# Kernel tuning notes

Measured on AMD Instinct MI355X. Metric: run time of the kernel, lower is better.

## Reference

```python
import jax, jax.numpy as jnp
import numpy as np

B, C, ANGRES, H, W = 4, 60, 5, 96, 96
N = ANGRES * ANGRES  # 25 angular views
D = C                # dims = channels in TrippleAttention


def _norm(x, axis):
    # torch F.normalize: x / max(||x||_2, 1e-12)
    n = jnp.linalg.norm(x, axis=axis, keepdims=True)
    return x / jnp.maximum(n, 1e-12)


def setup_inputs() -> dict:
    key = jax.random.key(0)
    ks = jax.random.split(key, 8)
    s = 0.02
    return {
        "x": jax.random.normal(ks[0], (B, C, N, H, W), jnp.float32),
        "w_spa_q": jax.random.normal(ks[1], (D, C), jnp.float32) * s,      # 1x1 conv, stride 1
        "w_spa_kv": jax.random.normal(ks[2], (2 * D, C), jnp.float32) * s, # 1x1 conv, stride 2
        "w_ang_qkv": jax.random.normal(ks[3], (3 * D, C), jnp.float32) * s,
        "w_fre_qkv": jax.random.normal(ks[4], (3 * D, C), jnp.float32) * s,
        "ln_gamma": jnp.ones((3 * D,), jnp.float32),
        "ln_beta": jnp.zeros((3 * D,), jnp.float32),
        "w_mlp1": jax.random.normal(ks[5], (C, 3 * D), jnp.float32) * s,   # torch Linear [out,in]
        "w_mlp2": jax.random.normal(ks[6], (C, C), jnp.float32) * s,
    }


def reference(x, w_spa_q, w_spa_kv, w_ang_qkv, w_fre_qkv, ln_gamma, ln_beta, w_mlp1, w_mlp2):
    b, c, n, h, w = x.shape
    d = w_spa_q.shape[0]

    # ---- SpatialAttention ----
    # q: stride-1 1x1 conv then '(b n) c h w -> b (h w) (c n)'
    sq = jnp.einsum('dc,bcnhw->bhwdn', w_spa_q, x).reshape(b, h * w, d * n)
    xs = x[:, :, :, ::2, ::2]                       # stride-2, kernel-1 conv == subsample
    h2, w2 = xs.shape[3], xs.shape[4]
    skv = jnp.einsum('dc,bcnhw->bdnhw', w_spa_kv, xs)
    sk = skv[:, :d].reshape(b, d * n, h2 * w2)       # 'b (c n) (h w)'
    sv = skv[:, d:].transpose(0, 3, 4, 1, 2).reshape(b, h2 * w2, d * n)  # 'b (h w) (c n)'
    sq = _norm(sq, -1)
    sk = _norm(sk, -2)
    s_att = jax.nn.softmax(sq @ sk, axis=-1)         # [b, hw, h2w2]
    s_fea = (s_att @ sv).reshape(b, h, w, d, n).transpose(0, 3, 4, 1, 2)  # [b,d,n,h,w]

    # ---- AngularAttention ----
    aqkv = jnp.einsum('dc,bcnhw->bdnhw', w_ang_qkv, x)
    aq = aqkv[:, :d].transpose(0, 2, 1, 3, 4).reshape(b, n, d * h * w)       # 'b (u v) (c h w)'
    ak = aqkv[:, d:2 * d].transpose(0, 1, 3, 4, 2).reshape(b, d * h * w, n)  # 'b (c h w) (u v)'
    av = aqkv[:, 2 * d:].transpose(0, 2, 1, 3, 4).reshape(b, n, d * h * w)
    aq = _norm(aq, -1)
    ak = _norm(ak, -2)
    a_att = jax.nn.softmax(aq @ ak, axis=-1)         # [b, n, n]
    a_fea = (a_att @ av).reshape(b, n, d, h, w).transpose(0, 2, 1, 3, 4)     # [b,d,n,h,w]

    # ---- FrequencyAttention (use_mask=False) ----
    fqkv = jnp.einsum('dc,bcnhw->bdnhw', w_fre_qkv, x)
    fq = fqkv[:, :d].reshape(b, d, n * h * w)        # 'b c (n h w)'
    fk = fqkv[:, d:2 * d].reshape(b, d, n * h * w).transpose(0, 2, 1)        # 'b (n h w) c'
    fv = fqkv[:, 2 * d:].reshape(b, d, n * h * w)
    fq = _norm(fq, -1)
    fk = _norm(fk, -2)
    f_att = jax.nn.softmax(fq @ fk, axis=-1)         # [b, d, d]
    f_fea = (f_att @ fv).reshape(b, d, n, h, w)

    # ---- concat + MLP (dropout is identity at inference) ----
    cat = jnp.concatenate([s_fea, a_fea, f_fea], axis=1)  # [b, 3d, n, h, w]
    t = cat.transpose(0, 3, 4, 2, 1)                      # [b, h, w, n, 3d]
    mu = t.mean(-1, keepdims=True)
    var = t.var(-1, keepdims=True)                        # biased var, matching torch LayerNorm
    t = (t - mu) / jnp.sqrt(var + 1e-5) * ln_gamma + ln_beta
    t = jax.nn.relu(t @ w_mlp1.T)
    t = t @ w_mlp2.T                                      # [b, h, w, n, c]
    return t.transpose(0, 4, 3, 1, 2) + x
```

## Files before the change

### kernel.cpp

```cpp
#include <hip/hip_runtime.h>
#include <hip/hip_bf16.h>

typedef unsigned short u16;
typedef float f32x4 __attribute__((ext_vector_type(4)));
typedef short s16x8 __attribute__((ext_vector_type(8)));


__device__ __forceinline__ float b2f(u16 u) {
  union { unsigned int i; float f; } v; v.i = ((unsigned int)u) << 16; return v.f;
}
__device__ __forceinline__ u16 f2b(float f) {
  union { float f; unsigned int i; } v; v.f = f;
  unsigned int i = v.i + 0x7FFFu + ((v.i >> 16) & 1u);
  return (u16)(i >> 16);
}

__global__ void fallback_copy(const float* __restrict__ x, float* __restrict__ out, size_t n) {
  size_t i = (size_t)blockIdx.x * 256 + threadIdx.x;
  size_t st = (size_t)gridDim.x * 256;
  for (; i < n; i += st) out[i] = x[i];
}

__global__ __launch_bounds__(256) void cast_x(const float* __restrict__ xb, u16* __restrict__ Xb) {
  size_t e = ((size_t)blockIdx.x * 256 + threadIdx.x) * 4;
  ushort4 o;
  if (e < 13824000) {
    float4 v = *(const float4*)(xb + e);
    o.x = f2b(v.x); o.y = f2b(v.y); o.z = f2b(v.z); o.w = f2b(v.w);
  } else { o.x = 0; o.y = 0; o.z = 0; o.w = 0; }
  *(ushort4*)(Xb + e) = o;
}

__global__ __launch_bounds__(256) void gram_gemm(const u16* __restrict__ Xall,
                                                 float* __restrict__ Pg) {
  __shared__ __align__(16) u16 As[128 * 40];
  __shared__ __align__(16) u16 Bs[128 * 40];
  const int z = blockIdx.z;
  const int b = z >> 1, kk = z & 1;
  const u16* A = Xall + (size_t)b * 14155776;
  float* C = Pg + (size_t)z * 2359296;
  const int tid = threadIdx.x;
  const int bm = blockIdx.x, bn = blockIdx.y;
  const int lane = tid & 63;
  const int wv = tid >> 6;
  const int wm = (wv >> 1) * 64, wn = (wv & 1) * 64;
  const int lm = lane & 15, lq = lane >> 4;
  f32x4 z4 = {0.f, 0.f, 0.f, 0.f};
  f32x4 acc[4][4];
#pragma unroll
  for (int i = 0; i < 4; ++i)
#pragma unroll
    for (int j = 0; j < 4; ++j) acc[i][j] = z4;

  const int kbeg = kk * 4608, kend = kbeg + 4608;
  for (int k0 = kbeg; k0 < kend; k0 += 32) {
    __syncthreads();
#pragma unroll
    for (int r = 0; r < 4; ++r) {
      int idx = tid + (r << 8);
      int row = (idx >> 2) & 127;
      int seg = idx & 3;
      if (r < 2) {
        const uint4* src = (const uint4*)(A + (size_t)(bm * 128 + row) * 9216 + k0 + seg * 8);
        *(uint4*)&As[row * 40 + seg * 8] = *src;
      } else {
        const uint4* src = (const uint4*)(A + (size_t)(bn * 128 + row) * 9216 + k0 + seg * 8);
        *(uint4*)&Bs[row * 40 + seg * 8] = *src;
      }
    }
    __syncthreads();
    s16x8 af[4], bf[4];
#pragma unroll
    for (int i = 0; i < 4; ++i)
      af[i] = *(const s16x8*)&As[(wm + i * 16 + lm) * 40 + lq * 8];
#pragma unroll
    for (int j = 0; j < 4; ++j)
      bf[j] = *(const s16x8*)&Bs[(wn + j * 16 + lm) * 40 + lq * 8];
#pragma unroll
    for (int i = 0; i < 4; ++i)
#pragma unroll
      for (int j = 0; j < 4; ++j)
        acc[i][j] = __builtin_amdgcn_mfma_f32_16x16x32_bf16(af[i], bf[j], acc[i][j], 0, 0, 0);
  }

#pragma unroll
  for (int i = 0; i < 4; ++i) {
    int row0 = bm * 128 + wm + i * 16 + lq * 4;
#pragma unroll
    for (int j = 0; j < 4; ++j) {
      int col = bn * 128 + wn + j * 16 + lm;
#pragma unroll
      for (int r = 0; r < 4; ++r)
        C[(size_t)(row0 + r) * 1536 + col] = acc[i][j][r];
    }
  }
}

__global__ __launch_bounds__(256) void reduce_g2(const float* __restrict__ Pg,
                                                 float* __restrict__ G2all) {
  int b = blockIdx.y;
  size_t r = ((size_t)blockIdx.x * 256 + threadIdx.x) * 4;
  float4 a = *(const float4*)(Pg + (size_t)(2 * b) * 2359296 + r);
  float4 c = *(const float4*)(Pg + (size_t)(2 * b + 1) * 2359296 + r);
  float4 o; o.x = a.x + c.x; o.y = a.y + c.y; o.z = a.z + c.z; o.w = a.w + c.w;
  *(float4*)(G2all + (size_t)b * 2359296 + r) = o;
}

__global__ __launch_bounds__(256) void proj_full(const float* __restrict__ xb,
    const float* __restrict__ Wq, const float* __restrict__ Wang,
    const float* __restrict__ Wfre, u16* __restrict__ PF) {
  int s = blockIdx.x * 256 + threadIdx.x;
  int grp = blockIdx.y;
  const float* W = (grp == 0) ? Wq : ((grp == 1) ? (Wang + 7200) : (Wfre + 7200));
  const float* xs = xb + s;
  float xr[60];
#pragma unroll
  for (int c = 0; c < 60; ++c) xr[c] = xs[(size_t)c * 230400];
  u16* ob = PF + (size_t)grp * 13824000 + s;
  for (int r0 = 0; r0 < 60; r0 += 4) {
    const float* w0 = W + r0 * 60;
    const float* w1 = w0 + 60;
    const float* w2 = w0 + 120;
    const float* w3 = w0 + 180;
    float a0 = 0.f, a1 = 0.f, a2 = 0.f, a3 = 0.f;
#pragma unroll
    for (int c = 0; c < 60; ++c) {
      float xv = xr[c];
      a0 += w0[c] * xv; a1 += w1[c] * xv; a2 += w2[c] * xv; a3 += w3[c] * xv;
    }
    ob[(size_t)(r0    ) * 230400] = f2b(a0);
    ob[(size_t)(r0 + 1) * 230400] = f2b(a1);
    ob[(size_t)(r0 + 2) * 230400] = f2b(a2);
    ob[(size_t)(r0 + 3) * 230400] = f2b(a3);
  }
}

__global__ __launch_bounds__(256) void proj_sub(const float* __restrict__ xb,
    const float* __restrict__ Wkv, u16* __restrict__ PS) {
  int s2 = blockIdx.x * 256 + threadIdx.x;
  int grp = blockIdx.y;
  int nn = s2 / 2304; int rem = s2 - nn * 2304;
  int hy = rem / 48;  int hx = rem - hy * 48;
  const float* xs = xb + (size_t)nn * 9216 + hy * 192 + hx * 2;
  float xr[60];
#pragma unroll
  for (int c = 0; c < 60; ++c) xr[c] = xs[(size_t)c * 230400];
  u16* ob = PS + (size_t)grp * 1728000 + s2;
  const float* Wg = Wkv + grp * 1800;
  for (int r0 = 0; r0 < 30; r0 += 5) {
    const float* w0 = Wg + r0 * 60;
    const float* w1 = w0 + 60;
    const float* w2 = w0 + 120;
    const float* w3 = w0 + 180;
    const float* w4 = w0 + 240;
    float a0 = 0.f, a1 = 0.f, a2 = 0.f, a3 = 0.f, a4 = 0.f;
#pragma unroll
    for (int c = 0; c < 60; ++c) {
      float xv = xr[c];
      a0 += w0[c] * xv; a1 += w1[c] * xv; a2 += w2[c] * xv;
      a3 += w3[c] * xv; a4 += w4[c] * xv;
    }
    ob[(size_t)(r0    ) * 57600] = f2b(a0);
    ob[(size_t)(r0 + 1) * 57600] = f2b(a1);
    ob[(size_t)(r0 + 2) * 57600] = f2b(a2);
    ob[(size_t)(r0 + 3) * 57600] = f2b(a3);
    ob[(size_t)(r0 + 4) * 57600] = f2b(a4);
  }
}

__global__ __launch_bounds__(256) void norm_sums(const u16* __restrict__ inb,
    float* __restrict__ partials, int S) {
  int s = blockIdx.x * 256 + threadIdx.x;
  int fc = blockIdx.y;
  const u16* p = inb + (size_t)(fc * 60) * S + s;
  float a0 = 0.f, a1 = 0.f, a2 = 0.f, a3 = 0.f;
#pragma unroll
  for (int f = 0; f < 60; f += 4) {
    float v0 = b2f(p[(size_t)(f + 0) * S]); a0 += v0 * v0;
    float v1 = b2f(p[(size_t)(f + 1) * S]); a1 += v1 * v1;
    float v2 = b2f(p[(size_t)(f + 2) * S]); a2 += v2 * v2;
    float v3 = b2f(p[(size_t)(f + 3) * S]); a3 += v3 * v3;
  }
  partials[(size_t)fc * S + s] = (a0 + a1) + (a2 + a3);
}

__global__ __launch_bounds__(256) void transpose_scale(const u16* __restrict__ inb,
    const float* __restrict__ partials, u16* __restrict__ outb, int S) {
  __shared__ float Ts[64 * 65];
  __shared__ float rinv[64];
  int s0 = blockIdx.x * 64, f0 = blockIdx.y * 64;
  int t = threadIdx.x; int sl = t & 63; int g = t >> 6;
  if (t < 64) {
    float tot = 0.f;
    for (int c = 0; c < 25; ++c) tot += partials[(size_t)c * S + s0 + t];
    rinv[t] = 1.f / fmaxf(sqrtf(tot), 1e-12f);
  }
  for (int e = t; e < 4096; e += 256) {
    int fr = e >> 6, sc = e & 63; int f = f0 + fr;
    Ts[fr * 65 + sc] = (f < 1500) ? b2f(inb[(size_t)f * S + s0 + sc]) : 0.f;
  }
  __syncthreads();
  for (int sr = g; sr < 64; sr += 4) {
    float v = Ts[sl * 65 + sr] * rinv[sr];
    outb[(size_t)(s0 + sr) * 1536 + f0 + sl] = f2b(v);
  }
}

template<int M, int N, int K, int EPI>
__global__ __launch_bounds__(256) void gemm_bt(const u16* __restrict__ A,
    const u16* __restrict__ BT, void* __restrict__ C) {
  __shared__ __align__(16) u16 As[128 * 40];
  __shared__ __align__(16) u16 Bs[128 * 40];
  const int tid = threadIdx.x;
  const int bm = blockIdx.x, bn = blockIdx.y;
  const int lane = tid & 63;
  const int wv = tid >> 6;
  const int wm = (wv >> 1) * 64, wn = (wv & 1) * 64;
  const int lm = lane & 15, lq = lane >> 4;
  f32x4 z = {0.f, 0.f, 0.f, 0.f};
  f32x4 acc[4][4];
#pragma unroll
  for (int i = 0; i < 4; ++i)
#pragma unroll
    for (int j = 0; j < 4; ++j) acc[i][j] = z;

  for (int k0 = 0; k0 < K; k0 += 32) {
    __syncthreads();
#pragma unroll
    for (int r = 0; r < 4; ++r) {
      int idx = tid + (r << 8);
      int row = (idx >> 2) & 127;
      int seg = idx & 3;
      if (r < 2) {
        const uint4* src = (const uint4*)(A + (size_t)(bm * 128 + row) * K + k0 + seg * 8);
        *(uint4*)&As[row * 40 + seg * 8] = *src;
      } else {
        const uint4* src = (const uint4*)(BT + (size_t)(bn * 128 + row) * K + k0 + seg * 8);
        *(uint4*)&Bs[row * 40 + seg * 8] = *src;
      }
    }
    __syncthreads();
    s16x8 af[4], bf[4];
#pragma unroll
    for (int i = 0; i < 4; ++i)
      af[i] = *(const s16x8*)&As[(wm + i * 16 + lm) * 40 + lq * 8];
#pragma unroll
    for (int j = 0; j < 4; ++j)
      bf[j] = *(const s16x8*)&Bs[(wn + j * 16 + lm) * 40 + lq * 8];
#pragma unroll
    for (int i = 0; i < 4; ++i)
#pragma unroll
      for (int j = 0; j < 4; ++j)
        acc[i][j] = __builtin_amdgcn_mfma_f32_16x16x32_bf16(af[i], bf[j], acc[i][j], 0, 0, 0);
  }

#pragma unroll
  for (int i = 0; i < 4; ++i) {
    int row0 = bm * 128 + wm + i * 16 + lq * 4;
#pragma unroll
    for (int j = 0; j < 4; ++j) {
      int col = bn * 128 + wn + j * 16 + lm;
      if (EPI == 0) {
        float* Cb = (float*)C;
#pragma unroll
        for (int r = 0; r < 4; ++r)
          Cb[(size_t)(row0 + r) * N + col] = acc[i][j][r];
      } else {
        if (col < 1500) {
          u16* Cb = (u16*)C;
          uint2 pk;
          pk.x = (unsigned int)f2b(acc[i][j][0]) | ((unsigned int)f2b(acc[i][j][1]) << 16);
          pk.y = (unsigned int)f2b(acc[i][j][2]) | ((unsigned int)f2b(acc[i][j][3]) << 16);
          *(uint2*)&Cb[(size_t)col * M + row0] = pk;
        }
      }
    }
  }
}

__global__ __launch_bounds__(256) void softmax_rows(const float* __restrict__ L,
                                                    u16* __restrict__ att) {
  size_t row = blockIdx.x;
  const float* Lr = L + row * 2304;
  u16* ar = att + row * 2304;
  int t = threadIdx.x;
  float v[9]; float mx = -1e30f;
#pragma unroll
  for (int i = 0; i < 9; ++i) { v[i] = Lr[t + i * 256]; mx = fmaxf(mx, v[i]); }
  __shared__ float red[256];
  red[t] = mx; __syncthreads();
  for (int st = 128; st > 0; st >>= 1) { if (t < st) red[t] = fmaxf(red[t], red[t + st]); __syncthreads(); }
  mx = red[0]; __syncthreads();
  float s = 0.f;
#pragma unroll
  for (int i = 0; i < 9; ++i) { v[i] = __expf(v[i] - mx); s += v[i]; }
  red[t] = s; __syncthreads();
  for (int st = 128; st > 0; st >>= 1) { if (t < st) red[t] += red[t + st]; __syncthreads(); }
  float rs = 1.f / red[0];
#pragma unroll
  for (int i = 0; i < 9; ++i) ar[t + i * 256] = f2b(v[i] * rs);
}

__global__ __launch_bounds__(256) void ang_dots(const float* __restrict__ G2all,
    const float* __restrict__ Ma_g, const float* __restrict__ Mq_g,
    const float* __restrict__ Mk_g, float* __restrict__ dotsAll) {
  int p = blockIdx.x;
  int b = blockIdx.y;
  const float* G = G2all + (size_t)b * 2359296;
  float* dots = dotsAll + b * 675;
  const float* m; int ri, ci;
  if (p < 625)      { m = Ma_g; ri = p / 25; ci = p % 25; }
  else if (p < 650) { m = Mq_g; ri = p - 625; ci = ri; }
  else              { m = Mk_g; ri = p - 650; ci = ri; }
  int t = threadIdx.x;
  float a = 0.f;
  for (int e = t; e < 3600; e += 256) {
    int c = e / 60, cp = e - c * 60;
    a += m[e] * G[(size_t)(c * 25 + ri) * 1536 + cp * 25 + ci];
  }
  __shared__ float red[256];
  red[t] = a; __syncthreads();
  for (int st = 128; st > 0; st >>= 1) { if (t < st) red[t] += red[t + st]; __syncthreads(); }
  if (t == 0) dots[p] = red[0];
}

__global__ __launch_bounds__(64) void ang_finish(const float* __restrict__ dotsAll,
                                                 float* __restrict__ AattAll) {
  int b = blockIdx.x;
  const float* dots = dotsAll + b * 675;
  float* Aatt = AattAll + b * 625;
  int t = threadIdx.x;
  if (t < 25) {
    float rq = 1.f / fmaxf(sqrtf(dots[625 + t]), 1e-12f);
    float l[25], mx = -1e30f;
    for (int j = 0; j < 25; ++j) {
      float rk = 1.f / fmaxf(sqrtf(dots[650 + j]), 1e-12f);
      l[j] = dots[t * 25 + j] * rq * rk;
      mx = fmaxf(mx, l[j]);
    }
    float s = 0.f;
    for (int j = 0; j < 25; ++j) { l[j] = __expf(l[j] - mx); s += l[j]; }
    float rs = 1.f / s;
    for (int j = 0; j < 25; ++j) Aatt[t * 25 + j] = l[j] * rs;
  }
}

__global__ __launch_bounds__(256) void fre_gs(const float* __restrict__ G2all,
                                              float* __restrict__ GsAll) {
  int e = blockIdx.x * 256 + threadIdx.x;
  int b = blockIdx.y;
  if (e >= 3600) return;
  const float* G = G2all + (size_t)b * 2359296;
  int c = e / 60, cp = e - c * 60;
  const float* base = G + (size_t)(c * 25) * 1536 + cp * 25;
  float a = 0.f;
#pragma unroll
  for (int n = 0; n < 25; ++n) a += base[(size_t)n * 1537];
  GsAll[b * 3600 + e] = a;
}

__global__ __launch_bounds__(256) void fre_finish(const float* __restrict__ GsAll,
    const float* __restrict__ Wfre, float* __restrict__ FattAll) {
  __shared__ float Gs[3600], T1q[3600], T1k[3600];
  __shared__ float qn[60], kn[60];
  int b = blockIdx.x;
  const float* Gs_g = GsAll + b * 3600;
  float* Fatt = FattAll + b * 3600;
  int t = threadIdx.x;
  for (int e = t; e < 3600; e += 256) Gs[e] = Gs_g[e];
  __syncthreads();
  for (int e = t; e < 3600; e += 256) {
    int u = e / 60, cp = e % 60;
    const float* wq = Wfre + u * 60;
    const float* wk = Wfre + 3600 + u * 60;
    float aq = 0.f, ak = 0.f;
    for (int c = 0; c < 60; ++c) { float g = Gs[c * 60 + cp]; aq += wq[c] * g; ak += wk[c] * g; }
    T1q[e] = aq; T1k[e] = ak;
  }
  __syncthreads();
  for (int e = t; e < 3600; e += 256) {
    int u = e / 60, v = e % 60;
    const float* wk = Wfre + 3600 + v * 60;
    float a = 0.f;
    for (int cp = 0; cp < 60; ++cp) a += T1q[u * 60 + cp] * wk[cp];
    Gs[e] = a;
  }
  for (int u = t; u < 60; u += 256) {
    const float* wq = Wfre + u * 60;
    const float* wk = Wfre + 3600 + u * 60;
    float aq = 0.f, ak = 0.f;
    for (int cp = 0; cp < 60; ++cp) { aq += T1q[u * 60 + cp] * wq[cp]; ak += T1k[u * 60 + cp] * wk[cp]; }
    qn[u] = aq; kn[u] = ak;
  }
  __syncthreads();
  if (t < 60) {
    float rq = 1.f / fmaxf(sqrtf(qn[t]), 1e-12f);
    float l[60], mx = -1e30f;
    for (int v = 0; v < 60; ++v) {
      float rk = 1.f / fmaxf(sqrtf(kn[v]), 1e-12f);
      l[v] = Gs[t * 60 + v] * rq * rk;
      mx = fmaxf(mx, l[v]);
    }
    float s = 0.f;
    for (int v = 0; v < 60; ++v) { l[v] = __expf(l[v] - mx); s += l[v]; }
    float rs = 1.f / s;
    for (int v = 0; v < 60; ++v) Fatt[t * 60 + v] = l[v] * rs;
  }
}

__global__ __launch_bounds__(256) void a_fea(const u16* __restrict__ PF,
    const float* __restrict__ Aatt, u16* __restrict__ CAT) {
  int hw = blockIdx.x * 256 + threadIdx.x;
  int dd = blockIdx.y;
  const u16* V = PF + ((size_t)(60 + dd)) * 230400 + hw;
  float v[25];
#pragma unroll
  for (int j = 0; j < 25; ++j) v[j] = b2f(V[(size_t)j * 9216]);
  u16* ob = CAT + (size_t)(1500 + dd * 25) * 9216 + hw;
  for (int i = 0; i < 25; ++i) {
    float a = 0.f;
#pragma unroll
    for (int j = 0; j < 25; ++j) a += Aatt[i * 25 + j] * v[j];
    ob[(size_t)i * 9216] = f2b(a);
  }
}

__global__ __launch_bounds__(256) void f_fea(const u16* __restrict__ PF,
    const float* __restrict__ Fatt, u16* __restrict__ CAT) {
  int s = blockIdx.x * 256 + threadIdx.x;
  const u16* V = PF + (size_t)120 * 230400 + s;
  float v[60];
#pragma unroll
  for (int u = 0; u < 60; ++u) v[u] = b2f(V[(size_t)u * 230400]);
  u16* ob = CAT + (size_t)27648000 + s;
  for (int u = 0; u < 60; ++u) {
    float a = 0.f;
#pragma unroll
    for (int vv = 0; vv < 60; ++vv) a += Fatt[u * 60 + vv] * v[vv];
    ob[(size_t)u * 230400] = f2b(a);
  }
}

__global__ void precompute(const float* __restrict__ W1, const float* __restrict__ W2,
    const float* __restrict__ gamma, const float* __restrict__ beta,
    const float* __restrict__ Wang,
    float* __restrict__ Avec, float* __restrict__ Btvec,
    float* __restrict__ W1T, float* __restrict__ W2T,
    float* __restrict__ Ma, float* __restrict__ Mq, float* __restrict__ Mk) {
  int t = threadIdx.x;
  for (int e = t; e < 10800; e += 256) { int q = e / 60, j = e % 60; W1T[e] = W1[j * 180 + q]; }
  for (int e = t; e < 3600;  e += 256) { int j = e / 60, k = e % 60; W2T[e] = W2[k * 60 + j]; }
  for (int e = t; e < 3600; e += 256) {
    int c = e / 60, cp = e % 60;
    const float* Waq = Wang;
    const float* Wak = Wang + 3600;
    float ma = 0.f, mq = 0.f, mk = 0.f;
    for (int d = 0; d < 60; ++d) {
      float q = Waq[d * 60 + c], qp = Waq[d * 60 + cp];
      float k = Wak[d * 60 + c], kp = Wak[d * 60 + cp];
      ma += q * kp; mq += q * qp; mk += k * kp;
    }
    Ma[e] = ma; Mq[e] = mq; Mk[e] = mk;
  }
  if (t < 60) {
    float a = 0.f, bt = 0.f;
    for (int q = 0; q < 180; ++q) { a += gamma[q] * W1[t * 180 + q]; bt += beta[q] * W1[t * 180 + q]; }
    Avec[t] = a; Btvec[t] = bt;
  }
}

__global__ __launch_bounds__(256) void fuse_ln_mlp(const u16* __restrict__ CAT,
    const float* __restrict__ xb, const float* __restrict__ gamma,
    const float* __restrict__ W1T, const float* __restrict__ W2T,
    const float* __restrict__ Avec, const float* __restrict__ Btvec,
    float* __restrict__ outb) {
  int s = blockIdx.x * 256 + threadIdx.x;
  const u16* cb = CAT + s;
  float S1[60];
#pragma unroll
  for (int j = 0; j < 60; ++j) S1[j] = 0.f;
  float sum = 0.f, sq = 0.f;
  for (int q = 0; q < 180; ++q) {
    float val = b2f(cb[(size_t)q * 230400]);
    sum += val; sq += val * val;
    float u = val * gamma[q];
    const float* w = W1T + q * 60;
#pragma unroll
    for (int j = 0; j < 60; ++j) S1[j] += u * w[j];
  }
  float mu = sum * (1.f / 180.f);
  float var = sq * (1.f / 180.f) - mu * mu;
  float inv = rsqrtf(var + 1e-5f);
  float y2[60];
#pragma unroll
  for (int k = 0; k < 60; ++k) y2[k] = 0.f;
  for (int j = 0; j < 60; ++j) {
    float y1 = inv * (S1[j] - mu * Avec[j]) + Btvec[j];
    y1 = fmaxf(y1, 0.f);
    const float* w = W2T + j * 60;
#pragma unroll
    for (int k = 0; k < 60; ++k) y2[k] += y1 * w[k];
  }
  const float* xs = xb + s;
  float* ob = outb + s;
#pragma unroll
  for (int k = 0; k < 60; ++k) ob[(size_t)k * 230400] = y2[k] + xs[(size_t)k * 230400];
}

extern "C" void kernel_launch(void* const* d_in, const int* in_sizes, int n_in,
                              void* d_out, int out_size, void* d_ws, size_t ws_size,
                              hipStream_t stream) {
  const float* x        = (const float*)d_in[0];
  const float* w_spa_q  = (const float*)d_in[1];
  const float* w_spa_kv = (const float*)d_in[2];
  const float* w_ang    = (const float*)d_in[3];
  const float* w_fre    = (const float*)d_in[4];
  const float* ln_gamma = (const float*)d_in[5];
  const float* ln_beta  = (const float*)d_in[6];
  const float* w_mlp1   = (const float*)d_in[7];
  const float* w_mlp2   = (const float*)d_in[8];
  float* out = (float*)d_out;
  (void)in_sizes; (void)n_in; (void)out_size;

  char* ws = (char*)d_ws;
  const size_t A1 = 0;
  const size_t A1_PS = 82944256;
  const size_t A2 = 96934656;
  const size_t A3 = 139401984;
  size_t off = 224336640;
  auto alloc = [&](size_t bytes) -> void* {
    void* p = ws + off; off = (off + bytes + 255) & ~(size_t)255; return p;
  };
  float* Aatt  = (float*)alloc(4 * 625 * 4);
  float* Fatt  = (float*)alloc(4 * 3600 * 4);
  float* Adots = (float*)alloc(4 * 675 * 4);
  float* Gsg   = (float*)alloc(4 * 3600 * 4);
  float* Avec  = (float*)alloc(240);
  float* Btvec = (float*)alloc(240);
  float* W1T   = (float*)alloc(43200);
  float* W2T   = (float*)alloc(14400);
  float* Ma    = (float*)alloc(14400);
  float* Mq    = (float*)alloc(14400);
  float* Mk    = (float*)alloc(14400);

  if (off > ws_size) {
    fallback_copy<<<4096, 256, 0, stream>>>(x, out, (size_t)55296000);
    return;
  }

  u16*   XbAll = (u16*)(ws);
  float* Pg    = (float*)(ws + 113246208);
  float* G2all = (float*)(ws);

  u16*   PF  = (u16*)(ws + A1);
  u16*   PS  = (u16*)(ws + A1_PS);
  u16*   sqn = (u16*)(ws + A2);
  u16*   skn = (u16*)(ws + A2 + 28311552);
  u16*   att = (u16*)(ws + A2);
  float* L   = (float*)(ws + A3);
  u16*   CAT = (u16*)(ws + A3);
  float* Pbig   = (float*)(ws + A3);
  float* Psmall = (float*)(ws + A3 + 921600);

  precompute<<<1, 256, 0, stream>>>(w_mlp1, w_mlp2, ln_gamma, ln_beta, w_ang,
                                    Avec, Btvec, W1T, W2T, Ma, Mq, Mk);

  for (int b = 0; b < 4; ++b)
    cast_x<<<13824, 256, 0, stream>>>(x + (size_t)b * 13824000, XbAll + (size_t)b * 14155776);
  gram_gemm<<<dim3(12, 12, 8), 256, 0, stream>>>(XbAll, Pg);
  reduce_g2<<<dim3(2304, 4), 256, 0, stream>>>(Pg, G2all);
  ang_dots<<<dim3(675, 4), 256, 0, stream>>>(G2all, Ma, Mq, Mk, Adots);
  ang_finish<<<4, 64, 0, stream>>>(Adots, Aatt);
  fre_gs<<<dim3(15, 4), 256, 0, stream>>>(G2all, Gsg);
  fre_finish<<<4, 256, 0, stream>>>(Gsg, w_fre, Fatt);

  for (int b = 0; b < 4; ++b) {
    const float* xb = x + (size_t)b * 13824000;
    float* outb = out + (size_t)b * 13824000;

    proj_full<<<dim3(900, 3), 256, 0, stream>>>(xb, w_spa_q, w_ang, w_fre, PF);
    proj_sub<<<dim3(225, 4), 256, 0, stream>>>(xb, w_spa_kv, PS);

    norm_sums<<<dim3(36, 25), 256, 0, stream>>>(PF, Pbig, 9216);
    transpose_scale<<<dim3(144, 24), 256, 0, stream>>>(PF, Pbig, sqn, 9216);
    norm_sums<<<dim3(9, 25), 256, 0, stream>>>(PS, Psmall, 2304);
    transpose_scale<<<dim3(36, 24), 256, 0, stream>>>(PS, Psmall, skn, 2304);

    gemm_bt<9216, 2304, 1536, 0><<<dim3(72, 18), 256, 0, stream>>>(sqn, skn, L);
    softmax_rows<<<9216, 256, 0, stream>>>(L, att);
    gemm_bt<9216, 1536, 2304, 2><<<dim3(72, 12), 256, 0, stream>>>(att, PS + 3456000, CAT);

    a_fea<<<dim3(36, 60), 256, 0, stream>>>(PF, Aatt + b * 625, CAT);
    f_fea<<<900, 256, 0, stream>>>(PF, Fatt + b * 3600, CAT);

    fuse_ln_mlp<<<900, 256, 0, stream>>>(CAT, xb, ln_gamma, W1T, W2T, Avec, Btvec, outb);
  }
}
```

Before: 3.725 ms.

## Exploit Gram matrix symmetry: compute upper-triangle tiles and mirror in reduce

```diff
diff --git a/kernel.cpp b/kernel.cpp
--- a/kernel.cpp
+++ b/kernel.cpp
@@ -39,8 +39,16 @@
   const int b = z >> 1, kk = z & 1;
   const u16* A = Xall + (size_t)b * 14155776;
   float* C = Pg + (size_t)z * 2359296;
+  {
+  }
+  int p = blockIdx.x;
+  int xcd = p & 7, loc = p >> 3;
+  int wg = (xcd < 6 ? xcd * 10 : 60 + (xcd - 6) * 9) + loc;
+  int bm = 0, rem = wg;
+  while (rem >= 12 - bm) { rem -= 12 - bm; ++bm; }
+  int bn = bm + rem;
+
   const int tid = threadIdx.x;
-  const int bm = blockIdx.x, bn = blockIdx.y;
   const int lane = tid & 63;
   const int wv = tid >> 6;
   const int wm = (wv >> 1) * 64, wn = (wv & 1) * 64;
@@ -96,14 +104,47 @@
   }
 }
 
-__global__ __launch_bounds__(256) void reduce_g2(const float* __restrict__ Pg,
-                                                 float* __restrict__ G2all) {
+__global__ __launch_bounds__(256) void reduce_mirror(const float* __restrict__ Pg,
+                                                     float* __restrict__ G2all) {
+  __shared__ float Ts[64 * 65];
   int b = blockIdx.y;
-  size_t r = ((size_t)blockIdx.x * 256 + threadIdx.x) * 4;
-  float4 a = *(const float4*)(Pg + (size_t)(2 * b) * 2359296 + r);
-  float4 c = *(const float4*)(Pg + (size_t)(2 * b + 1) * 2359296 + r);
-  float4 o; o.x = a.x + c.x; o.y = a.y + c.y; o.z = a.z + c.z; o.w = a.w + c.w;
-  *(float4*)(G2all + (size_t)b * 2359296 + r) = o;
+  int p = blockIdx.x;
+  int ti = 0, rem = p;
+  while (rem >= 24 - ti) { rem -= 24 - ti; ++ti; }
+  int tj = ti + rem;
+  const float* P0 = Pg + (size_t)(2 * b) * 2359296;
+  const float* P1 = P0 + 2359296;
+  float* G = G2all + (size_t)b * 2359296;
+  int t = threadIdx.x;
+  int r = t >> 4;
+  int c4 = (t & 15) * 4;
+#pragma unroll
+  for (int k = 0; k < 4; ++k) {
+    int rr = r + 16 * k;
+    size_t src = (size_t)(ti * 64 + rr) * 1536 + tj * 64 + c4;
+    float4 a = *(const float4*)(P0 + src);
+    float4 c = *(const float4*)(P1 + src);
+    float4 s; s.x = a.x + c.x; s.y = a.y + c.y; s.z = a.z + c.z; s.w = a.w + c.w;
+    *(float4*)(G + src) = s;
+    Ts[rr * 65 + c4 + 0] = s.x;
+    Ts[rr * 65 + c4 + 1] = s.y;
+    Ts[rr * 65 + c4 + 2] = s.z;
+    Ts[rr * 65 + c4 + 3] = s.w;
+  }
+  __syncthreads();
+  if (ti != tj) {
+#pragma unroll
+    for (int k = 0; k < 4; ++k) {
+      int rr = r + 16 * k;
+      size_t dst = (size_t)(tj * 64 + rr) * 1536 + ti * 64 + c4;
+      float4 s;
+      s.x = Ts[(c4 + 0) * 65 + rr];
+      s.y = Ts[(c4 + 1) * 65 + rr];
+      s.z = Ts[(c4 + 2) * 65 + rr];
+      s.w = Ts[(c4 + 3) * 65 + rr];
+      *(float4*)(G + dst) = s;
+    }
+  }
 }
 
 __global__ __launch_bounds__(256) void proj_full(const float* __restrict__ xb,
@@ -567,8 +608,8 @@
 
   for (int b = 0; b < 4; ++b)
     cast_x<<<13824, 256, 0, stream>>>(x + (size_t)b * 13824000, XbAll + (size_t)b * 14155776);
-  gram_gemm<<<dim3(12, 12, 8), 256, 0, stream>>>(XbAll, Pg);
-  reduce_g2<<<dim3(2304, 4), 256, 0, stream>>>(Pg, G2all);
+  gram_gemm<<<dim3(78, 1, 8), 256, 0, stream>>>(XbAll, Pg);
+  reduce_mirror<<<dim3(300, 4), 256, 0, stream>>>(Pg, G2all);
   ang_dots<<<dim3(675, 4), 256, 0, stream>>>(G2all, Ma, Mq, Mk, Adots);
   ang_finish<<<4, 64, 0, stream>>>(Adots, Aatt);
   fre_gs<<<dim3(15, 4), 256, 0, stream>>>(G2all, Gsg);
```

Measured after the change: 3.622 ms. -2.7%, faster.
